# Kernel tuning notes

Measured on AMD Instinct MI355X. Metric: run time of the kernel, lower is better.

The kernel has to match this reference:

```python
import jax, jax.numpy as jnp
import numpy as np

B, D, H = 128, 256, 512  # batch, input_size, hidden_size; 2 hidden layers
ORDER = 'A'
EPS = 1e-12


def _masks():
    # Standard MADE sequential degrees: inputs 1..D (reversed for order 'B'),
    # hidden degrees cycle over 1..D-1. Hidden mask: >=, output mask: > (strict).
    din = np.arange(1, D + 1) if ORDER == 'A' else np.arange(D, 0, -1)
    dh = (np.arange(H) % (D - 1)) + 1
    m0 = (dh[:, None] >= din[None, :]).astype(np.float32)  # [H, D]
    m1 = (dh[:, None] >= dh[None, :]).astype(np.float32)   # [H, H]
    mo = (din[:, None] > dh[None, :]).astype(np.float32)   # [D, H]
    return jnp.asarray(m0), jnp.asarray(m1), jnp.asarray(mo)


def _made(y, W0, b0, W1, b1, Wo, bo, masks):
    m0, m1, mo = masks
    h = jax.nn.elu(y @ (W0 * m0).T + b0)   # [B, H]
    h = jax.nn.elu(h @ (W1 * m1).T + b1)   # [B, H]
    return h @ (Wo * mo).T + bo            # [B, D]


def setup_inputs() -> dict:
    key = jax.random.key(0)
    ks = jax.random.split(key, 13)
    s_in, s_h = 1.0 / np.sqrt(D), 1.0 / np.sqrt(H)

    def p(k, shape, s):
        return (jax.random.normal(k, shape, jnp.float32) * s).astype(jnp.float32)

    return {
        'x': jax.random.normal(ks[0], (B, D), jnp.float32),
        'mu_W0': p(ks[1], (H, D), s_in), 'mu_b0': jnp.zeros((H,), jnp.float32),
        'mu_W1': p(ks[2], (H, H), s_h),  'mu_b1': jnp.zeros((H,), jnp.float32),
        'mu_Wo': p(ks[3], (D, H), s_h),  'mu_bo': jnp.zeros((D,), jnp.float32),
        'lv_W0': p(ks[4], (H, D), s_in), 'lv_b0': jnp.zeros((H,), jnp.float32),
        'lv_W1': p(ks[5], (H, H), s_h),  'lv_b1': jnp.zeros((H,), jnp.float32),
        'lv_Wo': p(ks[6], (D, H), s_h),  'lv_bo': jnp.zeros((D,), jnp.float32),
    }


def reference(x, mu_W0, mu_b0, mu_W1, mu_b1, mu_Wo, mu_bo,
              lv_W0, lv_b0, lv_W1, lv_b1, lv_Wo, lv_bo):
    masks = _masks()
    idx = jnp.arange(D) if ORDER == 'A' else jnp.arange(D - 1, -1, -1)

    def step(carry, i):
        y, _ = carry
        mu = _made(y, mu_W0, mu_b0, mu_W1, mu_b1, mu_Wo, mu_bo, masks)
        logstd = 0.5 * _made(y, lv_W0, lv_b0, lv_W1, lv_b1, lv_Wo, lv_bo, masks)
        new_col = (x[:, i] - mu[:, i]) / (jnp.exp(logstd[:, i]) + EPS)
        y = y.at[:, i].set(new_col)
        return (y, logstd), None

    init = (jnp.zeros_like(x), jnp.zeros_like(x))
    (y, logstd), _ = jax.lax.scan(step, init, idx)
    return y, logstd.sum(axis=1)
```

## Files before the change

kernel.cpp:

```cpp
#include <hip/hip_runtime.h>

#define DD 256
#define HH 512
#define BB 128
#define TS 4096

#define WAITVM(N) asm volatile("s_waitcnt vmcnt(" #N ")" ::: "memory")
#define SYNC() do { __builtin_amdgcn_s_barrier(); __builtin_amdgcn_sched_barrier(0); } while (0)

__device__ __forceinline__ float elu_f(float x) {
    return x > 0.f ? x : (__expf(x) - 1.f);
}
__device__ __forceinline__ float rlf(float v, int l) {
    return __uint_as_float(__builtin_amdgcn_readlane(__float_as_uint(v), (unsigned)l));
}
__device__ __forceinline__ float f4c(const float4& v, int r) {
    return r == 0 ? v.x : r == 1 ? v.y : r == 2 ? v.z : v.w;
}

__device__ __forceinline__ int pmap(int h) {
    if (h == 510) return 255;
    if (h == 511) return 511;
    return (h < 255) ? (4 * (h & 63) + (h >> 6))
                     : (256 + 4 * ((h - 255) & 63) + ((h - 255) >> 6));
}
__device__ __forceinline__ int p4map(int j) {
    return 4 * (j & 63) + (j >> 6);
}
__device__ __forceinline__ int w1base(int hp) {
    return (hp <= 254) ? hp * TS
         : (hp <= 509) ? (hp - 255) * TS + 1024
         : 255 * TS + ((hp == 510) ? 0 : 1024);
}
__device__ __forceinline__ int wobase(int hp) {
    return (hp <= 254) ? hp * TS + 3072
         : (hp <= 509) ? (hp - 255) * TS + 3584
         : 255 * TS + ((hp == 510) ? 2048 : 2560);
}

__global__ __launch_bounds__(256) void prep(
    const float* __restrict__ w0m_, const float* __restrict__ w0l_,
    const float* __restrict__ w1m_, const float* __restrict__ w1l_,
    const float* __restrict__ wom_, const float* __restrict__ wol_,
    float* __restrict__ tape)
{
    __shared__ float tm[32][33], tl[32][33];
    const int tx = threadIdx.x & 31, ty = threadIdx.x >> 5;
    const unsigned b = blockIdx.x;

    if (b < 256) {
        const int h0 = (int)(b >> 4) << 5, hp0 = (int)(b & 15) << 5;
        #pragma unroll
        for (int j = 0; j < 4; ++j) {
            int r = ty + 8 * j;
            tm[r][tx] = w1m_[(h0 + r) * HH + hp0 + tx];
            tl[r][tx] = w1l_[(h0 + r) * HH + hp0 + tx];
        }
        __syncthreads();
        #pragma unroll
        for (int j = 0; j < 4; ++j) {
            int hp = hp0 + ty + 8 * j;
            int h  = h0 + tx;
            int dh_h = (h <= 254) ? h + 1 : (h <= 509 ? h - 254 : h - 509);
            int dh_p = (hp <= 254) ? hp + 1 : (hp <= 509 ? hp - 254 : hp - 509);
            float mask = (dh_h >= dh_p) ? 1.f : 0.f;
            int base = w1base(hp), p = pmap(h);
            tape[base + p]       = mask * tm[tx][ty + 8 * j];
            tape[base + 512 + p] = mask * tl[tx][ty + 8 * j];
        }
    } else if (b < 384) {
        const int b2 = (int)b - 256;
        const int h0 = (b2 >> 3) << 5, i0 = (b2 & 7) << 5;
        #pragma unroll
        for (int j = 0; j < 4; ++j) {
            int r = ty + 8 * j;
            tm[r][tx] = w0m_[(h0 + r) * DD + i0 + tx];
            tl[r][tx] = w0l_[(h0 + r) * DD + i0 + tx];
        }
        __syncthreads();
        #pragma unroll
        for (int j = 0; j < 4; ++j) {
            int i = i0 + ty + 8 * j;
            int h = h0 + tx;
            int p = pmap(h);
            tape[i * TS + 2048 + p] = tm[tx][ty + 8 * j];
            tape[i * TS + 2560 + p] = tl[tx][ty + 8 * j];
        }
    } else {
        const int b3 = (int)b - 384;
        const int j0 = (b3 >> 4) << 5, hp0 = (b3 & 15) << 5;
        #pragma unroll
        for (int j = 0; j < 4; ++j) {
            int r = ty + 8 * j;
            tm[r][tx] = wom_[(j0 + r) * HH + hp0 + tx];
            tl[r][tx] = wol_[(j0 + r) * HH + hp0 + tx];
        }
        __syncthreads();
        #pragma unroll
        for (int j = 0; j < 4; ++j) {
            int hp = hp0 + ty + 8 * j;
            int jj = j0 + tx;
            int base = wobase(hp), p = p4map(jj);
            tape[base + p]       = tm[tx][ty + 8 * j];
            tape[base + 256 + p] = tl[tx][ty + 8 * j];
        }
    }
}

struct WSet { float4 w[16]; };

__device__ __forceinline__ void stage16(const float* g, float* l, int lane) {
    #pragma unroll
    for (int k = 0; k < 16; ++k) {
        __builtin_amdgcn_global_load_lds(
            (const __attribute__((address_space(1))) void*)(g + 256 * k + 4 * lane),
            (__attribute__((address_space(3))) void*)(l + 256 * k),
            16, 0, 0);
    }
}

__device__ __forceinline__ void rd_set(WSet& S, const float* b, int lane) {
    const float4* p = (const float4*)b;
    #pragma unroll
    for (int k = 0; k < 16; ++k) S.w[k] = p[64 * k + lane];
}

template<int Q, int EX>
__device__ __forceinline__ void stepC(
    int t, int lane, const WSet& S,
    float (&a0m)[8], float (&a0l)[8], float (&a1m)[8], float (&a1l)[8],
    float (&Rm)[4], float (&Rl)[4], float (&yv)[4],
    const float (&xv)[4], const float (&bmv)[4], const float (&blv)[4],
    float& ls_sum,
    const float4& exmA, const float4& exmB, const float4& exlA, const float4& exlB,
    const float4& exwm, const float4& exwl)
{
    float mu = rlf(Rm[Q], t) + rlf(bmv[Q], t);
    float ls = 0.5f * (rlf(Rl[Q], t) + rlf(blv[Q], t));
    ls_sum += ls;
    float v = __fdividef(rlf(xv[Q], t) - mu, __expf(ls) + 1e-12f);
    yv[Q] = (lane == t) ? v : yv[Q];

    #pragma unroll
    for (int r = Q; r < 4; ++r) {
        a0m[r]     += v * f4c(S.w[8], r);
        a0m[4 + r] += v * f4c(S.w[9], r);
        a0l[r]     += v * f4c(S.w[10], r);
        a0l[4 + r] += v * f4c(S.w[11], r);
    }

    float p0m = elu_f(rlf(a0m[Q], t)),     p0l = elu_f(rlf(a0l[Q], t));
    float p1m = elu_f(rlf(a0m[4 + Q], t)), p1l = elu_f(rlf(a0l[4 + Q], t));
    float p2m = 0.f, p2l = 0.f;
    if (EX) {
        p2m = elu_f(rlf(a0m[EX == 1 ? 3 : 7], 63));
        p2l = elu_f(rlf(a0l[EX == 1 ? 3 : 7], 63));
    }

    #pragma unroll
    for (int r = Q; r < 4; ++r) {
        a1m[r]     += f4c(S.w[0], r) * p0m + f4c(S.w[4], r) * p1m;
        a1m[4 + r] += f4c(S.w[1], r) * p0m + f4c(S.w[5], r) * p1m;
        a1l[r]     += f4c(S.w[2], r) * p0l + f4c(S.w[6], r) * p1l;
        a1l[4 + r] += f4c(S.w[3], r) * p0l + f4c(S.w[7], r) * p1l;
    }
    if (EX) {
        #pragma unroll
        for (int r = 0; r < 4; ++r) {
            a1m[r]     += f4c(exmA, r) * p2m;
            a1m[4 + r] += f4c(exmB, r) * p2m;
            a1l[r]     += f4c(exlA, r) * p2l;
            a1l[4 + r] += f4c(exlB, r) * p2l;
        }
    }

    float q0m = elu_f(rlf(a1m[Q], t)),     q0l = elu_f(rlf(a1l[Q], t));
    float q1m = elu_f(rlf(a1m[4 + Q], t)), q1l = elu_f(rlf(a1l[4 + Q], t));
    float q2m = 0.f, q2l = 0.f;
    if (EX) {
        q2m = elu_f(rlf(a1m[EX == 1 ? 3 : 7], 63));
        q2l = elu_f(rlf(a1l[EX == 1 ? 3 : 7], 63));
    }

    #pragma unroll
    for (int r = Q; r < 4; ++r) {
        Rm[r] += f4c(S.w[12], r) * q0m + f4c(S.w[14], r) * q1m;
        Rl[r] += f4c(S.w[13], r) * q0l + f4c(S.w[15], r) * q1l;
    }
    if (EX) {
        #pragma unroll
        for (int r = 0; r < 4; ++r) {
            Rm[r] += f4c(exwm, r) * q2m;
            Rl[r] += f4c(exwl, r) * q2l;
        }
    }
}

__global__ __launch_bounds__(128, 1) void made_main(
    const float* __restrict__ x,
    const float* __restrict__ mu_b0, const float* __restrict__ mu_b1,
    const float* __restrict__ mu_bo,
    const float* __restrict__ lv_b0, const float* __restrict__ lv_b1,
    const float* __restrict__ lv_bo,
    const float* __restrict__ tape,
    float* __restrict__ out)
{
    __shared__ __align__(16) float buf[4][TS];
    const int row = blockIdx.x;

    if (threadIdx.x >= 64) {
        const int lane = threadIdx.x - 64;
        #pragma unroll
        for (int g = 0; g < 3; ++g)
            stage16(tape + (size_t)g * TS, &buf[g][0], lane);
        #pragma unroll 1
        for (int t = 0; t < 255; ++t) {
            WAITVM(32);
            __builtin_amdgcn_s_barrier();
            __builtin_amdgcn_sched_barrier(0);
            int g = t + 3;
            if (g < 255)
                stage16(tape + (size_t)g * TS, &buf[g & 3][0], lane);
        }
        return;
    }

    const int lane = threadIdx.x;

    float a0m[8], a0l[8], a1m[8], a1l[8], Rm[4], Rl[4], yv[4];
    float xv[4], bmv[4], blv[4];
    #pragma unroll
    for (int r = 0; r < 4; ++r) {
        a0m[r]     = mu_b0[lane + 64 * r];
        a0m[4 + r] = mu_b0[255 + lane + 64 * r];
        a0l[r]     = lv_b0[lane + 64 * r];
        a0l[4 + r] = lv_b0[255 + lane + 64 * r];
        a1m[r]     = mu_b1[lane + 64 * r];
        a1m[4 + r] = mu_b1[255 + lane + 64 * r];
        a1l[r]     = lv_b1[lane + 64 * r];
        a1l[4 + r] = lv_b1[255 + lane + 64 * r];
        Rm[r] = 0.f; Rl[r] = 0.f; yv[r] = 0.f;
        xv[r]  = x[row * DD + 64 * r + lane];
        bmv[r] = mu_bo[64 * r + lane];
        blv[r] = lv_bo[64 * r + lane];
    }
    if (lane == 63) {
        a0m[3] = mu_b0[510]; a0m[7] = mu_b0[511];
        a0l[3] = lv_b0[510]; a0l[7] = lv_b0[511];
        a1m[3] = mu_b1[510]; a1m[7] = mu_b1[511];
        a1l[3] = lv_b1[510]; a1l[7] = lv_b1[511];
    }

    const float4* a4 = (const float4*)(tape + 255 * TS);
    float4 e510mA = a4[lane],       e510mB = a4[64 + lane];
    float4 e510lA = a4[128 + lane], e510lB = a4[192 + lane];
    float4 e511mA = a4[256 + lane], e511mB = a4[320 + lane];
    float4 e511lA = a4[384 + lane], e511lB = a4[448 + lane];
    float4 wo510m = a4[512 + lane], wo510l = a4[576 + lane];
    float4 wo511m = a4[640 + lane], wo511l = a4[704 + lane];

    const float4 d4 = make_float4(0.f, 0.f, 0.f, 0.f);

    float ls_sum = 0.f;

    SYNC();
    {
        WSet S; rd_set(S, &buf[0][0], lane);
        stepC<0, 1>(0, lane, S, a0m, a0l, a1m, a1l, Rm, Rl, yv, xv, bmv, blv,
                    ls_sum, e510mA, e510mB, e510lA, e510lB, wo510m, wo510l);
    }

    SYNC();
    {
        WSet S; rd_set(S, &buf[1][0], lane);
        stepC<0, 2>(1, lane, S, a0m, a0l, a1m, a1l, Rm, Rl, yv, xv, bmv, blv,
                    ls_sum, e511mA, e511mB, e511lA, e511lB, wo511m, wo511l);
    }

#define STEP_BODY(Q, t, tl)                                                   \
    {                                                                         \
        SYNC();                                                               \
        WSet S; rd_set(S, &buf[(t) & 3][0], lane);                            \
        stepC<Q, 0>((tl), lane, S, a0m, a0l, a1m, a1l, Rm, Rl, yv,            \
                    xv, bmv, blv, ls_sum, d4, d4, d4, d4, d4, d4);            \
    }

    #pragma unroll 1
    for (int t = 2; t < 64; ++t)    STEP_BODY(0, t, t)
    #pragma unroll 1
    for (int t = 64; t < 128; ++t)  STEP_BODY(1, t, t - 64)
    #pragma unroll 1
    for (int t = 128; t < 192; ++t) STEP_BODY(2, t, t - 128)
    #pragma unroll 1
    for (int t = 192; t < 255; ++t) STEP_BODY(3, t, t - 192)
#undef STEP_BODY

    {
        float mu = rlf(Rm[3], 63) + rlf(bmv[3], 63);
        float ls = 0.5f * (rlf(Rl[3], 63) + rlf(blv[3], 63));
        ls_sum += ls;
        float v = __fdividef(rlf(xv[3], 63) - mu, __expf(ls) + 1e-12f);
        yv[3] = (lane == 63) ? v : yv[3];
    }

    #pragma unroll
    for (int r = 0; r < 4; ++r) out[row * DD + 64 * r + lane] = yv[r];
    if (lane == 0) out[BB * DD + row] = ls_sum;
}

extern "C" void kernel_launch(void* const* d_in, const int* in_sizes, int n_in,
                              void* d_out, int out_size, void* d_ws, size_t ws_size,
                              hipStream_t stream) {
    const float* x     = (const float*)d_in[0];
    const float* mu_W0 = (const float*)d_in[1];
    const float* mu_b0 = (const float*)d_in[2];
    const float* mu_W1 = (const float*)d_in[3];
    const float* mu_b1 = (const float*)d_in[4];
    const float* mu_Wo = (const float*)d_in[5];
    const float* mu_bo = (const float*)d_in[6];
    const float* lv_W0 = (const float*)d_in[7];
    const float* lv_b0 = (const float*)d_in[8];
    const float* lv_W1 = (const float*)d_in[9];
    const float* lv_b1 = (const float*)d_in[10];
    const float* lv_Wo = (const float*)d_in[11];
    const float* lv_bo = (const float*)d_in[12];

    float* tape = (float*)d_ws;

    prep<<<512, 256, 0, stream>>>(mu_W0, lv_W0, mu_W1, lv_W1, mu_Wo, lv_Wo, tape);
    made_main<<<BB, 128, 0, stream>>>(x, mu_b0, mu_b1, mu_bo,
                                      lv_b0, lv_b1, lv_bo, tape, (float*)d_out);
}
```

Baseline: 185.2 us.

## Double-buffer LDS weight-set reads one step ahead of compute

The compute wave now keeps two register weight sets and issues the LDS reads for step t+1 before running step t's compute, with the loop unrolled by two to alternate the sets. The producer waves wait for one fewer outstanding staging group, so each tape slice is ready a step earlier to support the prefetch. This aims to hide LDS read latency behind the serial per-step arithmetic. In exchange it roughly doubles the registers held for weights, which may cause spills, and it tightens the margin in the four-slot staging ring.

```diff
diff --git a/kernel.cpp b/kernel.cpp
--- a/kernel.cpp
+++ b/kernel.cpp
@@ -215,7 +215,7 @@
             stage16(tape + (size_t)g * TS, &buf[g][0], lane);
         #pragma unroll 1
         for (int t = 0; t < 255; ++t) {
-            WAITVM(32);
+            if (t < 253) { WAITVM(16); } else { WAITVM(0); }
             __builtin_amdgcn_s_barrier();
             __builtin_amdgcn_sched_barrier(0);
             int g = t + 3;
@@ -262,38 +262,44 @@
     const float4 d4 = make_float4(0.f, 0.f, 0.f, 0.f);
 
     float ls_sum = 0.f;
+    WSet A, B;
 
     SYNC();
-    {
-        WSet S; rd_set(S, &buf[0][0], lane);
-        stepC<0, 1>(0, lane, S, a0m, a0l, a1m, a1l, Rm, Rl, yv, xv, bmv, blv,
-                    ls_sum, e510mA, e510mB, e510lA, e510lB, wo510m, wo510l);
-    }
+    rd_set(A, &buf[0][0], lane);
+    rd_set(B, &buf[1][0], lane);
+    stepC<0, 1>(0, lane, A, a0m, a0l, a1m, a1l, Rm, Rl, yv, xv, bmv, blv,
+                ls_sum, e510mA, e510mB, e510lA, e510lB, wo510m, wo510l);
 
     SYNC();
-    {
-        WSet S; rd_set(S, &buf[1][0], lane);
-        stepC<0, 2>(1, lane, S, a0m, a0l, a1m, a1l, Rm, Rl, yv, xv, bmv, blv,
-                    ls_sum, e511mA, e511mB, e511lA, e511lB, wo511m, wo511l);
-    }
-
-#define STEP_BODY(Q, t, tl)                                                   \
+    rd_set(A, &buf[2][0], lane);
+    stepC<0, 2>(1, lane, B, a0m, a0l, a1m, a1l, Rm, Rl, yv, xv, bmv, blv,
+                ls_sum, e511mA, e511mB, e511lA, e511lB, wo511m, wo511l);
+
+#define PAIR_BODY(Q, t, tl)                                                   \
     {                                                                         \
         SYNC();                                                               \
-        WSet S; rd_set(S, &buf[(t) & 3][0], lane);                            \
-        stepC<Q, 0>((tl), lane, S, a0m, a0l, a1m, a1l, Rm, Rl, yv,            \
+        rd_set(B, &buf[((t) + 1) & 3][0], lane);                              \
+        stepC<Q, 0>((tl), lane, A, a0m, a0l, a1m, a1l, Rm, Rl, yv,            \
                     xv, bmv, blv, ls_sum, d4, d4, d4, d4, d4, d4);            \
+        SYNC();                                                               \
+        rd_set(A, &buf[((t) + 2) & 3][0], lane);                              \
+        stepC<Q, 0>((tl) + 1, lane, B, a0m, a0l, a1m, a1l, Rm, Rl, yv,        \
+                    xv, bmv, blv, ls_sum, d4, d4, d4, d4, d4, d4);            \
     }
 
     #pragma unroll 1
-    for (int t = 2; t < 64; ++t)    STEP_BODY(0, t, t)
+    for (int t = 2; t < 64; t += 2)    PAIR_BODY(0, t, t)
     #pragma unroll 1
-    for (int t = 64; t < 128; ++t)  STEP_BODY(1, t, t - 64)
+    for (int t = 64; t < 128; t += 2)  PAIR_BODY(1, t, t - 64)
     #pragma unroll 1
-    for (int t = 128; t < 192; ++t) STEP_BODY(2, t, t - 128)
+    for (int t = 128; t < 192; t += 2) PAIR_BODY(2, t, t - 128)
     #pragma unroll 1
-    for (int t = 192; t < 255; ++t) STEP_BODY(3, t, t - 192)
-#undef STEP_BODY
+    for (int t = 192; t < 254; t += 2) PAIR_BODY(3, t, t - 192)
+#undef PAIR_BODY
+
+    SYNC();
+    stepC<3, 0>(62, lane, A, a0m, a0l, a1m, a1l, Rm, Rl, yv, xv, bmv, blv,
+                ls_sum, d4, d4, d4, d4, d4, d4);
 
     {
         float mu = rlf(Rm[3], 63) + rlf(bmv[3], 63);
```

After: 183.1 us. No clear change (-1.1%).

## Replace LDS producer-wave pipeline with register-level quad-buffered global prefetch

Applied to the files above, without the earlier changes.

Drops the second producer wave and the shared-memory ring buffer, which staged per-step weight tapes with global_load_lds plus a barrier every step. The single compute wave now loads each step's weights straight into registers three steps ahead, using four rotating register sets and vmcnt waits. This removes per-step LDS round trips and barriers. In exchange it uses far more VGPRs (four 64-float sets) and relies on the exact vmcnt counting to stay correct.

```diff
diff --git a/kernel.cpp b/kernel.cpp
--- a/kernel.cpp
+++ b/kernel.cpp
@@ -6,7 +6,6 @@
 #define TS 4096
 
 #define WAITVM(N) asm volatile("s_waitcnt vmcnt(" #N ")" ::: "memory")
-#define SYNC() do { __builtin_amdgcn_s_barrier(); __builtin_amdgcn_sched_barrier(0); } while (0)
 
 __device__ __forceinline__ float elu_f(float x) {
     return x > 0.f ? x : (__expf(x) - 1.f);
@@ -109,18 +108,8 @@
 
 struct WSet { float4 w[16]; };
 
-__device__ __forceinline__ void stage16(const float* g, float* l, int lane) {
-    #pragma unroll
-    for (int k = 0; k < 16; ++k) {
-        __builtin_amdgcn_global_load_lds(
-            (const __attribute__((address_space(1))) void*)(g + 256 * k + 4 * lane),
-            (__attribute__((address_space(3))) void*)(l + 256 * k),
-            16, 0, 0);
-    }
-}
-
-__device__ __forceinline__ void rd_set(WSet& S, const float* b, int lane) {
-    const float4* p = (const float4*)b;
+__device__ __forceinline__ void ld_issue(WSet& S, const float* g, int lane) {
+    const float4* p = (const float4*)g;
     #pragma unroll
     for (int k = 0; k < 16; ++k) S.w[k] = p[64 * k + lane];
 }
@@ -196,7 +185,7 @@
     }
 }
 
-__global__ __launch_bounds__(128, 1) void made_main(
+__global__ __launch_bounds__(64, 1) void made_main(
     const float* __restrict__ x,
     const float* __restrict__ mu_b0, const float* __restrict__ mu_b1,
     const float* __restrict__ mu_bo,
@@ -205,26 +194,7 @@
     const float* __restrict__ tape,
     float* __restrict__ out)
 {
-    __shared__ __align__(16) float buf[4][TS];
     const int row = blockIdx.x;
-
-    if (threadIdx.x >= 64) {
-        const int lane = threadIdx.x - 64;
-        #pragma unroll
-        for (int g = 0; g < 3; ++g)
-            stage16(tape + (size_t)g * TS, &buf[g][0], lane);
-        #pragma unroll 1
-        for (int t = 0; t < 255; ++t) {
-            WAITVM(32);
-            __builtin_amdgcn_s_barrier();
-            __builtin_amdgcn_sched_barrier(0);
-            int g = t + 3;
-            if (g < 255)
-                stage16(tape + (size_t)g * TS, &buf[g & 3][0], lane);
-        }
-        return;
-    }
-
     const int lane = threadIdx.x;
 
     float a0m[8], a0l[8], a1m[8], a1l[8], Rm[4], Rl[4], yv[4];
@@ -261,39 +231,76 @@
 
     const float4 d4 = make_float4(0.f, 0.f, 0.f, 0.f);
 
+    WSet W0, W1, W2, W3;
+    ld_issue(W0, tape + 0 * TS, lane);
+    ld_issue(W1, tape + 1 * TS, lane);
+    ld_issue(W2, tape + 2 * TS, lane);
+
     float ls_sum = 0.f;
 
-    SYNC();
-    {
-        WSet S; rd_set(S, &buf[0][0], lane);
-        stepC<0, 1>(0, lane, S, a0m, a0l, a1m, a1l, Rm, Rl, yv, xv, bmv, blv,
-                    ls_sum, e510mA, e510mB, e510lA, e510lB, wo510m, wo510l);
-    }
-
-    SYNC();
-    {
-        WSet S; rd_set(S, &buf[1][0], lane);
-        stepC<0, 2>(1, lane, S, a0m, a0l, a1m, a1l, Rm, Rl, yv, xv, bmv, blv,
-                    ls_sum, e511mA, e511mB, e511lA, e511lB, wo511m, wo511l);
-    }
-
-#define STEP_BODY(Q, t, tl)                                                   \
+    ld_issue(W3, tape + 3 * TS, lane);
+    WAITVM(32);
+    stepC<0, 1>(0, lane, W0, a0m, a0l, a1m, a1l, Rm, Rl, yv, xv, bmv, blv,
+                ls_sum, e510mA, e510mB, e510lA, e510lB, wo510m, wo510l);
+
+    ld_issue(W0, tape + 4 * TS, lane);
+    WAITVM(32);
+    stepC<0, 2>(1, lane, W1, a0m, a0l, a1m, a1l, Rm, Rl, yv, xv, bmv, blv,
+                ls_sum, e511mA, e511mB, e511lA, e511lB, wo511m, wo511l);
+
+#define SSTEP(Q, tt, WC, WN)                                                  \
     {                                                                         \
-        SYNC();                                                               \
-        WSet S; rd_set(S, &buf[(t) & 3][0], lane);                            \
-        stepC<Q, 0>((tl), lane, S, a0m, a0l, a1m, a1l, Rm, Rl, yv,            \
-                    xv, bmv, blv, ls_sum, d4, d4, d4, d4, d4, d4);            \
+        ld_issue(WN, tape + (size_t)((tt) + 3) * TS, lane);                   \
+        WAITVM(32);                                                           \
+        stepC<Q, 0>((tt) - 64 * (Q), lane, WC, a0m, a0l, a1m, a1l,            \
+                    Rm, Rl, yv, xv, bmv, blv, ls_sum,                         \
+                    d4, d4, d4, d4, d4, d4);                                  \
     }
 
     #pragma unroll 1
-    for (int t = 2; t < 64; ++t)    STEP_BODY(0, t, t)
+    for (int t = 2; t < 62; t += 4) {
+        SSTEP(0, t,     W2, W1)
+        SSTEP(0, t + 1, W3, W2)
+        SSTEP(0, t + 2, W0, W3)
+        SSTEP(0, t + 3, W1, W0)
+    }
+    SSTEP(0, 62, W2, W1)
+    SSTEP(0, 63, W3, W2)
+
     #pragma unroll 1
-    for (int t = 64; t < 128; ++t)  STEP_BODY(1, t, t - 64)
+    for (int t = 64; t < 128; t += 4) {
+        SSTEP(1, t,     W0, W3)
+        SSTEP(1, t + 1, W1, W0)
+        SSTEP(1, t + 2, W2, W1)
+        SSTEP(1, t + 3, W3, W2)
+    }
+
     #pragma unroll 1
-    for (int t = 128; t < 192; ++t) STEP_BODY(2, t, t - 128)
+    for (int t = 128; t < 192; t += 4) {
+        SSTEP(2, t,     W0, W3)
+        SSTEP(2, t + 1, W1, W0)
+        SSTEP(2, t + 2, W2, W1)
+        SSTEP(2, t + 3, W3, W2)
+    }
+
     #pragma unroll 1
-    for (int t = 192; t < 255; ++t) STEP_BODY(3, t, t - 192)
-#undef STEP_BODY
+    for (int t = 192; t < 252; t += 4) {
+        SSTEP(3, t,     W0, W3)
+        SSTEP(3, t + 1, W1, W0)
+        SSTEP(3, t + 2, W2, W1)
+        SSTEP(3, t + 3, W3, W2)
+    }
+#undef SSTEP
+
+    WAITVM(32);
+    stepC<3, 0>(60, lane, W0, a0m, a0l, a1m, a1l, Rm, Rl, yv, xv, bmv, blv,
+                ls_sum, d4, d4, d4, d4, d4, d4);
+    WAITVM(16);
+    stepC<3, 0>(61, lane, W1, a0m, a0l, a1m, a1l, Rm, Rl, yv, xv, bmv, blv,
+                ls_sum, d4, d4, d4, d4, d4, d4);
+    WAITVM(0);
+    stepC<3, 0>(62, lane, W2, a0m, a0l, a1m, a1l, Rm, Rl, yv, xv, bmv, blv,
+                ls_sum, d4, d4, d4, d4, d4, d4);
 
     {
         float mu = rlf(Rm[3], 63) + rlf(bmv[3], 63);
@@ -328,6 +335,6 @@
     float* tape = (float*)d_ws;
 
     prep<<<512, 256, 0, stream>>>(mu_W0, lv_W0, mu_W1, lv_W1, mu_Wo, lv_Wo, tape);
-    made_main<<<BB, 128, 0, stream>>>(x, mu_b0, mu_b1, mu_bo,
-                                      lv_b0, lv_b1, lv_bo, tape, (float*)d_out);
-}
+    made_main<<<BB, 64, 0, stream>>>(x, mu_b0, mu_b1, mu_bo,
+                                     lv_b0, lv_b1, lv_bo, tape, (float*)d_out);
+}
```

Result: slower. 234.6 us (+26.7%).

## Drop producer wave; single wave self-prefetches weight tape with vmcnt waits

Applied to the files above, without the earlier changes.

Removes the separate 64-thread producer wave and the per-step workgroup barriers. The compute wave now issues its own global-to-LDS prefetch of the tape three steps ahead and waits only on vmcnt. It also computes the next step's output value at the end of each step and reorders the LDS reads so the first-used weights arrive first. The aim is to take barrier latency off the serial 255-step critical path. In exchange, issuing the async loads costs compute-wave instructions, and the pipeline now depends on correct vmcnt counting for LDS visibility without a barrier.

```diff
diff --git a/kernel.cpp b/kernel.cpp
--- a/kernel.cpp
+++ b/kernel.cpp
@@ -6,7 +6,6 @@
 #define TS 4096
 
 #define WAITVM(N) asm volatile("s_waitcnt vmcnt(" #N ")" ::: "memory")
-#define SYNC() do { __builtin_amdgcn_s_barrier(); __builtin_amdgcn_sched_barrier(0); } while (0)
 
 __device__ __forceinline__ float elu_f(float x) {
     return x > 0.f ? x : (__expf(x) - 1.f);
@@ -119,26 +118,33 @@
     }
 }
 
-__device__ __forceinline__ void rd_set(WSet& S, const float* b, int lane) {
+__device__ __forceinline__ void rd_use(WSet& S, const float* b, int lane) {
     const float4* p = (const float4*)b;
-    #pragma unroll
-    for (int k = 0; k < 16; ++k) S.w[k] = p[64 * k + lane];
+    const int ord[16] = {8, 9, 10, 11, 0, 4, 1, 5, 2, 6, 3, 7, 12, 14, 13, 15};
+    #pragma unroll
+    for (int k = 0; k < 16; ++k) S.w[ord[k]] = p[64 * ord[k] + lane];
+}
+
+template<int QN>
+__device__ __forceinline__ float nextV(
+    int tn, const float (&Rm)[4], const float (&Rl)[4],
+    const float (&xv)[4], const float (&bmv)[4], const float (&blv)[4],
+    float& ls_sum)
+{
+    float mu = rlf(Rm[QN], tn) + rlf(bmv[QN], tn);
+    float ls = 0.5f * (rlf(Rl[QN], tn) + rlf(blv[QN], tn));
+    ls_sum += ls;
+    return __fdividef(rlf(xv[QN], tn) - mu, __expf(ls) + 1e-12f);
 }
 
 template<int Q, int EX>
-__device__ __forceinline__ void stepC(
-    int t, int lane, const WSet& S,
+__device__ __forceinline__ void stepC_v(
+    int t, int lane, float v, const WSet& S,
     float (&a0m)[8], float (&a0l)[8], float (&a1m)[8], float (&a1l)[8],
     float (&Rm)[4], float (&Rl)[4], float (&yv)[4],
-    const float (&xv)[4], const float (&bmv)[4], const float (&blv)[4],
-    float& ls_sum,
     const float4& exmA, const float4& exmB, const float4& exlA, const float4& exlB,
     const float4& exwm, const float4& exwl)
 {
-    float mu = rlf(Rm[Q], t) + rlf(bmv[Q], t);
-    float ls = 0.5f * (rlf(Rl[Q], t) + rlf(blv[Q], t));
-    ls_sum += ls;
-    float v = __fdividef(rlf(xv[Q], t) - mu, __expf(ls) + 1e-12f);
     yv[Q] = (lane == t) ? v : yv[Q];
 
     #pragma unroll
@@ -196,7 +202,7 @@
     }
 }
 
-__global__ __launch_bounds__(128, 1) void made_main(
+__global__ __launch_bounds__(64, 1) void made_main(
     const float* __restrict__ x,
     const float* __restrict__ mu_b0, const float* __restrict__ mu_b1,
     const float* __restrict__ mu_bo,
@@ -207,24 +213,6 @@
 {
     __shared__ __align__(16) float buf[4][TS];
     const int row = blockIdx.x;
-
-    if (threadIdx.x >= 64) {
-        const int lane = threadIdx.x - 64;
-        #pragma unroll
-        for (int g = 0; g < 3; ++g)
-            stage16(tape + (size_t)g * TS, &buf[g][0], lane);
-        #pragma unroll 1
-        for (int t = 0; t < 255; ++t) {
-            WAITVM(32);
-            __builtin_amdgcn_s_barrier();
-            __builtin_amdgcn_sched_barrier(0);
-            int g = t + 3;
-            if (g < 255)
-                stage16(tape + (size_t)g * TS, &buf[g & 3][0], lane);
-        }
-        return;
-    }
-
     const int lane = threadIdx.x;
 
     float a0m[8], a0l[8], a1m[8], a1l[8], Rm[4], Rl[4], yv[4];
@@ -261,47 +249,74 @@
 
     const float4 d4 = make_float4(0.f, 0.f, 0.f, 0.f);
 
+    stage16(tape + 0 * TS, &buf[0][0], lane);
+    stage16(tape + 1 * TS, &buf[1][0], lane);
+    stage16(tape + 2 * TS, &buf[2][0], lane);
+
     float ls_sum = 0.f;
-
-    SYNC();
+    WSet S;
+
+    float v = nextV<0>(0, Rm, Rl, xv, bmv, blv, ls_sum);
+
+    WAITVM(32);
+    rd_use(S, &buf[0][0], lane);
+    stage16(tape + 3 * TS, &buf[3][0], lane);
+    stepC_v<0, 1>(0, lane, v, S, a0m, a0l, a1m, a1l, Rm, Rl, yv,
+                  e510mA, e510mB, e510lA, e510lB, wo510m, wo510l);
+    v = nextV<0>(1, Rm, Rl, xv, bmv, blv, ls_sum);
+
+    WAITVM(32);
+    rd_use(S, &buf[1][0], lane);
+    stage16(tape + 4 * TS, &buf[0][0], lane);
+    stepC_v<0, 2>(1, lane, v, S, a0m, a0l, a1m, a1l, Rm, Rl, yv,
+                  e511mA, e511mB, e511lA, e511lB, wo511m, wo511l);
+    v = nextV<0>(2, Rm, Rl, xv, bmv, blv, ls_sum);
+
+#define SSTEP(Q, tt, QN, tn)                                                  \
+    {                                                                         \
+        WAITVM(32);                                                           \
+        rd_use(S, &buf[(tt) & 3][0], lane);                                   \
+        if ((tt) + 3 < 255)                                                   \
+            stage16(tape + (size_t)((tt) + 3) * TS,                           \
+                    &buf[((tt) + 3) & 3][0], lane);                           \
+        stepC_v<Q, 0>((tt) - 64 * (Q), lane, v, S, a0m, a0l, a1m, a1l,        \
+                      Rm, Rl, yv, d4, d4, d4, d4, d4, d4);                    \
+        v = nextV<QN>((tn), Rm, Rl, xv, bmv, blv, ls_sum);                    \
+    }
+
+    #pragma unroll 1
+    for (int t = 2; t < 63; ++t) SSTEP(0, t, 0, t + 1)
+    SSTEP(0, 63, 1, 0)
+
+    #pragma unroll 1
+    for (int t = 64; t < 127; ++t) SSTEP(1, t, 1, t - 63)
+    SSTEP(1, 127, 2, 0)
+
+    #pragma unroll 1
+    for (int t = 128; t < 191; ++t) SSTEP(2, t, 2, t - 127)
+    SSTEP(2, 191, 3, 0)
+
+    #pragma unroll 1
+    for (int t = 192; t < 252; ++t) SSTEP(3, t, 3, t - 191)
+    SSTEP(3, 252, 3, 61)
+
     {
-        WSet S; rd_set(S, &buf[0][0], lane);
-        stepC<0, 1>(0, lane, S, a0m, a0l, a1m, a1l, Rm, Rl, yv, xv, bmv, blv,
-                    ls_sum, e510mA, e510mB, e510lA, e510lB, wo510m, wo510l);
-    }
-
-    SYNC();
+        WAITVM(16);
+        rd_use(S, &buf[253 & 3][0], lane);
+        stepC_v<3, 0>(61, lane, v, S, a0m, a0l, a1m, a1l, Rm, Rl, yv,
+                      d4, d4, d4, d4, d4, d4);
+        v = nextV<3>(62, Rm, Rl, xv, bmv, blv, ls_sum);
+    }
     {
-        WSet S; rd_set(S, &buf[1][0], lane);
-        stepC<0, 2>(1, lane, S, a0m, a0l, a1m, a1l, Rm, Rl, yv, xv, bmv, blv,
-                    ls_sum, e511mA, e511mB, e511lA, e511lB, wo511m, wo511l);
-    }
-
-#define STEP_BODY(Q, t, tl)                                                   \
-    {                                                                         \
-        SYNC();                                                               \
-        WSet S; rd_set(S, &buf[(t) & 3][0], lane);                            \
-        stepC<Q, 0>((tl), lane, S, a0m, a0l, a1m, a1l, Rm, Rl, yv,            \
-                    xv, bmv, blv, ls_sum, d4, d4, d4, d4, d4, d4);            \
-    }
-
-    #pragma unroll 1
-    for (int t = 2; t < 64; ++t)    STEP_BODY(0, t, t)
-    #pragma unroll 1
-    for (int t = 64; t < 128; ++t)  STEP_BODY(1, t, t - 64)
-    #pragma unroll 1
-    for (int t = 128; t < 192; ++t) STEP_BODY(2, t, t - 128)
-    #pragma unroll 1
-    for (int t = 192; t < 255; ++t) STEP_BODY(3, t, t - 192)
-#undef STEP_BODY
-
-    {
-        float mu = rlf(Rm[3], 63) + rlf(bmv[3], 63);
-        float ls = 0.5f * (rlf(Rl[3], 63) + rlf(blv[3], 63));
-        ls_sum += ls;
-        float v = __fdividef(rlf(xv[3], 63) - mu, __expf(ls) + 1e-12f);
-        yv[3] = (lane == 63) ? v : yv[3];
-    }
+        WAITVM(0);
+        rd_use(S, &buf[254 & 3][0], lane);
+        stepC_v<3, 0>(62, lane, v, S, a0m, a0l, a1m, a1l, Rm, Rl, yv,
+                      d4, d4, d4, d4, d4, d4);
+        v = nextV<3>(63, Rm, Rl, xv, bmv, blv, ls_sum);
+    }
+#undef SSTEP
+
+    yv[3] = (lane == 63) ? v : yv[3];
 
     #pragma unroll
     for (int r = 0; r < 4; ++r) out[row * DD + 64 * r + lane] = yv[r];
@@ -328,6 +343,6 @@
     float* tape = (float*)d_ws;
 
     prep<<<512, 256, 0, stream>>>(mu_W0, lv_W0, mu_W1, lv_W1, mu_Wo, lv_Wo, tape);
-    made_main<<<BB, 128, 0, stream>>>(x, mu_b0, mu_b1, mu_bo,
-                                      lv_b0, lv_b1, lv_bo, tape, (float*)d_out);
-}
+    made_main<<<BB, 64, 0, stream>>>(x, mu_b0, mu_b1, mu_bo,
+                                     lv_b0, lv_b1, lv_bo, tape, (float*)d_out);
+}
```

After: 246.7 us. 33.2% more time.
